# Kernel tuning notes

Measured on AMD Instinct MI355X. Metric: run time of the kernel, lower is better.

The kernel has to match this reference:

```python
import jax, jax.numpy as jnp
import numpy as np

N = 50000      # graph nodes
E = 400000     # random edges (plus N self-loops)
F = 128        # graph feature dim
H = 4          # GAT heads (layer1)
DH = 64        # gnn_hidden_size (per-head out, layer1)
EMB = 8        # emb_size / GAT final out
B = 16384      # batch
NS = 20        # number of sparse features
V = 1000       # vocab per sparse feature
DENSE = 64     # num_fea_size
HID = 256      # hidden_dims
EPS = 1e-5


def setup_inputs():
    key = jax.random.key(0)
    ks = jax.random.split(key, 40)
    loop = jnp.arange(N, dtype=jnp.int32)
    src = jnp.concatenate([jax.random.randint(ks[0], (E,), 0, N, dtype=jnp.int32), loop])
    dst = jnp.concatenate([jax.random.randint(ks[1], (E,), 0, N, dtype=jnp.int32), loop])
    s = 0.05
    d = {
        'X_id': jax.random.randint(ks[2], (B, 2), 0, N),
        'X_sparse': jax.random.randint(ks[3], (B, NS), 0, V),
        'X_dense': jax.random.normal(ks[4], (B, DENSE), jnp.float32),
        'emb_tables': jax.random.normal(ks[5], (NS, V, EMB), jnp.float32) * s,
        'graph_feature': jax.random.normal(ks[6], (N, F), jnp.float32),
        'src': src, 'dst': dst,
        'wide_w': jax.random.normal(ks[7], (EMB, DENSE), jnp.float32) * s,
        'wide_b': jnp.zeros((EMB,), jnp.float32),
        'lin1_w': jax.random.normal(ks[8], (HID, NS * EMB + DENSE), jnp.float32) * s,
        'lin1_b': jnp.zeros((HID,), jnp.float32),
        'bn1_g': jnp.ones((HID,), jnp.float32),
        'bn1_b': jnp.zeros((HID,), jnp.float32),
        'bn1_m': jax.random.normal(ks[9], (HID,), jnp.float32) * s,
        'bn1_v': jnp.ones((HID,), jnp.float32),
        'lin2_w': jax.random.normal(ks[10], (HID, HID), jnp.float32) * s,
        'lin2_b': jnp.zeros((HID,), jnp.float32),
        'bn2_g': jnp.ones((HID,), jnp.float32),
        'bn2_b': jnp.zeros((HID,), jnp.float32),
        'bn2_m': jax.random.normal(ks[11], (HID,), jnp.float32) * s,
        'bn2_v': jnp.ones((HID,), jnp.float32),
        'dnn_w': jax.random.normal(ks[12], (EMB, HID), jnp.float32) * s,
        'dnn_b': jnp.zeros((EMB,), jnp.float32),
        'gat1_w': jax.random.normal(ks[13], (H * DH, F), jnp.float32) * s,
        'gat1_al': jax.random.normal(ks[14], (H, DH), jnp.float32) * s,
        'gat1_ar': jax.random.normal(ks[15], (H, DH), jnp.float32) * s,
        'gat1_bias': jnp.zeros((H * DH,), jnp.float32),
        'gat2_w': jax.random.normal(ks[16], (EMB, H * DH), jnp.float32) * s,
        'gat2_al': jax.random.normal(ks[17], (1, EMB), jnp.float32) * s,
        'gat2_ar': jax.random.normal(ks[18], (1, EMB), jnp.float32) * s,
        'gat2_bias': jnp.zeros((EMB,), jnp.float32),
        'g1w': jax.random.normal(ks[19], (1, EMB), jnp.float32) * s,
        'g1b': jnp.zeros((1,), jnp.float32),
        'g2w': jax.random.normal(ks[20], (1, EMB), jnp.float32) * s,
        'g2b': jnp.zeros((1,), jnp.float32),
        'g3w': jax.random.normal(ks[21], (1, EMB), jnp.float32) * s,
        'g3b': jnp.zeros((1,), jnp.float32),
        'gout_w': jax.random.normal(ks[22], (2, 3 * EMB), jnp.float32) * s,
        'gout_b': jnp.zeros((2,), jnp.float32),
    }
    return d


def gat_conv(h, W, al, ar, bias, src, dst, heads, dh):
    # DGL GATConv: project, per-edge attention, edge-softmax over dst, aggregate
    feat = (h @ W.T).reshape(-1, heads, dh)          # [N, H, D]
    el = (feat * al).sum(-1)                          # [N, H] src score
    er = (feat * ar).sum(-1)                          # [N, H] dst score
    e = jax.nn.leaky_relu(el[src] + er[dst], 0.2)     # [Etot, H]
    emax = jax.lax.stop_gradient(jax.ops.segment_max(e, dst, num_segments=N))
    a = jnp.exp(e - emax[dst])
    denom = jax.ops.segment_sum(a, dst, num_segments=N)  # [N, H]
    alpha = a / denom[dst]                            # [Etot, H]
    out = jax.ops.segment_sum(alpha[:, :, None] * feat[src], dst, num_segments=N)
    return out + bias.reshape(1, heads, dh)           # [N, H, D]


def batchnorm_eval(x, g, b, m, v):
    return g * (x - m) * jax.lax.rsqrt(v + EPS) + b


def reference(X_id, X_sparse, X_dense, emb_tables, graph_feature, src, dst,
              wide_w, wide_b, lin1_w, lin1_b, bn1_g, bn1_b, bn1_m, bn1_v,
              lin2_w, lin2_b, bn2_g, bn2_b, bn2_m, bn2_v, dnn_w, dnn_b,
              gat1_w, gat1_al, gat1_ar, gat1_bias, gat2_w, gat2_al, gat2_ar, gat2_bias,
              g1w, g1b, g2w, g2b, g3w, g3b, gout_w, gout_b):
    commit_ids = X_id[:, 1]
    # sparse embedding lookup: [B, NS, EMB] -> [B, NS*EMB]
    sparse_embed = emb_tables[jnp.arange(NS)[None, :], X_sparse].reshape(B, NS * EMB)
    x = jnp.concatenate([sparse_embed, X_dense], axis=-1)
    wide_out = X_dense @ wide_w.T + wide_b            # [B, EMB]
    # deep MLP (eval-mode BN, dropout = identity)
    d = jax.nn.relu(batchnorm_eval(x @ lin1_w.T + lin1_b, bn1_g, bn1_b, bn1_m, bn1_v))
    d = jax.nn.relu(batchnorm_eval(d @ lin2_w.T + lin2_b, bn2_g, bn2_b, bn2_m, bn2_v))
    deep_out = d @ dnn_w.T + dnn_b                    # [B, EMB]
    # GAT
    h1 = gat_conv(graph_feature, gat1_w, gat1_al, gat1_ar, gat1_bias, src, dst, H, DH)
    h1 = jax.nn.elu(h1.reshape(N, H * DH))
    h2 = gat_conv(h1, gat2_w, gat2_al, gat2_ar, gat2_bias, src, dst, 1, EMB)
    gcn = h2.reshape(N, EMB)                          # squeeze head dim
    gcn_out = gcn[commit_ids]                         # [B, EMB]
    # Gate (concat)
    aw = jax.nn.sigmoid(wide_out @ g1w.T + g1b)
    bw = jax.nn.sigmoid(deep_out @ g2w.T + g2b)
    cw = jax.nn.sigmoid(gcn_out @ g3w.T + g3b)
    tot = aw + bw + cw
    combined = jnp.concatenate([(aw / tot) * wide_out, (bw / tot) * deep_out,
                                (cw / tot) * gcn_out], axis=1)
    out = combined @ gout_w.T + gout_b                # [B, 2]
    return jax.nn.softmax(out, axis=1)
```

## Files before the change

kernel.cpp:

```cpp
#include <hip/hip_runtime.h>

#define TPB 256
#define DCAP 64
constexpr float BN_EPS = 1e-5f;

typedef __attribute__((ext_vector_type(8))) short short8;
typedef __attribute__((ext_vector_type(4))) float floatx4;

__device__ __forceinline__ float sigmoidf_(float x) { return 1.f / (1.f + __expf(-x)); }
__device__ __forceinline__ unsigned short f2bf(float f) {
    unsigned u = __float_as_uint(f);
    u += 0x7FFFu + ((u >> 16) & 1u);
    return (unsigned short)(u >> 16);
}
__device__ __forceinline__ float bf2f(unsigned short h) {
    return __uint_as_float((unsigned)h << 16);
}
__device__ __forceinline__ float bflo(unsigned v) { return __uint_as_float(v << 16); }
__device__ __forceinline__ float bfhi(unsigned v) { return __uint_as_float(v & 0xFFFF0000u); }

__device__ __forceinline__ void async_load16(const unsigned short* g, unsigned short* l) {
    __builtin_amdgcn_global_load_lds(
        (const __attribute__((address_space(1))) void*)g,
        (__attribute__((address_space(3))) void*)l, 16, 0, 0);
}

template<bool BNRELU, bool ATTN>
__device__ __forceinline__ void gemm_dev(
    const unsigned short* __restrict__ A, const unsigned short* __restrict__ W,
    const float* __restrict__ bias,
    const float* __restrict__ g, const float* __restrict__ bb,
    const float* __restrict__ bm, const float* __restrict__ bv,
    unsigned short* __restrict__ C, int M, int N, int K, int m0, int n0,
    unsigned short* As, unsigned short* Bs,
    const float* __restrict__ al = nullptr, const float* __restrict__ ar = nullptr,
    float* __restrict__ el = nullptr, float* __restrict__ er = nullptr)
{
    constexpr int SK = 32;
    int tid = threadIdx.x;
    int wave = tid >> 6, lane = tid & 63;
    int wm = (wave & 1) * 32, wn = (wave >> 1) * 32;
    int lrow = lane & 15, lk = (lane >> 4) * 8;
    int sr = tid >> 2, sc = (tid & 3) * 8;
    int gmA = m0 + sr; if (gmA >= M) gmA = M - 1;
    const unsigned short* gA = A + (size_t)gmA * K + sc;
    const unsigned short* gB = W + (size_t)(n0 + sr) * K + sc;
    unsigned short* lA = As + wave * 512;
    unsigned short* lB = Bs + wave * 512;
    floatx4 acc[2][2] = {};
    for (int k0 = 0; k0 < K; k0 += 32) {
        async_load16(gA + k0, lA);
        async_load16(gB + k0, lB);
        __syncthreads();
        short8 af[2], bfr[2];
#pragma unroll
        for (int i = 0; i < 2; ++i)
            af[i] = *(const short8*)(As + (wm + i * 16 + lrow) * SK + lk);
#pragma unroll
        for (int j = 0; j < 2; ++j)
            bfr[j] = *(const short8*)(Bs + (wn + j * 16 + lrow) * SK + lk);
#pragma unroll
        for (int i = 0; i < 2; ++i)
#pragma unroll
            for (int j = 0; j < 2; ++j)
                acc[i][j] = __builtin_amdgcn_mfma_f32_16x16x32_bf16(
                    af[i], bfr[j], acc[i][j], 0, 0, 0);
        __syncthreads();
    }
    int crow = (lane >> 4) * 4, ccol = lane & 15;
    float pl[2][4], pr[2][4];
    if (ATTN) {
#pragma unroll
        for (int i = 0; i < 2; ++i)
#pragma unroll
            for (int r = 0; r < 4; ++r) { pl[i][r] = 0.f; pr[i][r] = 0.f; }
    }
#pragma unroll
    for (int j = 0; j < 2; ++j) {
        int gn = n0 + wn + j * 16 + ccol;
        float sc2 = 1.f, sh = 0.f;
        if (BNRELU) {
            sc2 = g[gn] * rsqrtf(bv[gn] + BN_EPS);
            sh = (bias[gn] - bm[gn]) * sc2 + bb[gn];
        }
        float alv = 0.f, arv = 0.f;
        if (ATTN) { alv = al[gn]; arv = ar[gn]; }
#pragma unroll
        for (int i = 0; i < 2; ++i) {
#pragma unroll
            for (int r = 0; r < 4; ++r) {
                int gm = m0 + wm + i * 16 + crow + r;
                float t = acc[i][j][r];
                if (BNRELU) t = fmaxf(t * sc2 + sh, 0.f);
                unsigned short tb = f2bf(t);
                if (gm < M) C[(size_t)gm * N + gn] = tb;
                if (ATTN) {
                    float tf = bf2f(tb);
                    pl[i][r] += tf * alv;
                    pr[i][r] += tf * arv;
                }
            }
        }
    }
    if (ATTN) {
#pragma unroll
        for (int off = 1; off < 16; off <<= 1)
#pragma unroll
            for (int i = 0; i < 2; ++i)
#pragma unroll
                for (int r = 0; r < 4; ++r) {
                    pl[i][r] += __shfl_xor(pl[i][r], off, 16);
                    pr[i][r] += __shfl_xor(pr[i][r], off, 16);
                }
        float* scr = (float*)As;
        if (ccol == 0) {
#pragma unroll
            for (int i = 0; i < 2; ++i)
#pragma unroll
                for (int r = 0; r < 4; ++r) {
                    int row = wm + i * 16 + crow + r;
                    scr[(row * 2 + (wn >> 5)) * 2 + 0] = pl[i][r];
                    scr[(row * 2 + (wn >> 5)) * 2 + 1] = pr[i][r];
                }
        }
        __syncthreads();
        if (tid < 64) {
            int gm = m0 + tid;
            if (gm < M) {
                float e_l = scr[(tid * 2 + 0) * 2 + 0] + scr[(tid * 2 + 1) * 2 + 0];
                float e_r = scr[(tid * 2 + 0) * 2 + 1] + scr[(tid * 2 + 1) * 2 + 1];
                int h = n0 >> 6;
                el[(size_t)gm * 4 + h] = e_l;
                er[(size_t)gm * 4 + h] = e_r;
            }
        }
    }
}

__global__ __launch_bounds__(TPB) void stageA_kernel(
    const int* __restrict__ src, const int* __restrict__ dst,
    int* __restrict__ cnt, int* __restrict__ esrc, int E, int sblk,
    const float* __restrict__ w1, unsigned short* __restrict__ o1,
    const float* __restrict__ w2, unsigned short* __restrict__ o2,
    const float* __restrict__ w3, unsigned short* __restrict__ o3,
    const float* __restrict__ gfeat, unsigned short* __restrict__ gfeatb, int ng4,
    const int* __restrict__ Xs, const float* __restrict__ Xd,
    const float* __restrict__ emb, unsigned short* __restrict__ x, int nx, int pblk,
    const float* __restrict__ Ww, const float* __restrict__ wb,
    float* __restrict__ wide, int B)
{
    if ((int)blockIdx.x < sblk) {
        int i = blockIdx.x * TPB + threadIdx.x;
        if (i >= E) return;
        int d = dst[i];
        int pos = atomicAdd(&cnt[d], 1);
        if (pos < DCAP) esrc[(size_t)d * DCAP + pos] = src[i];
        return;
    }
    if ((int)blockIdx.x < sblk + pblk) {
        const int NW = 256 * 224 + 256 * 256 + 256 * 128;
        int idx = (blockIdx.x - sblk) * TPB + threadIdx.x;
        if (idx < NW) {
            if (idx < 256 * 224) o1[idx] = f2bf(w1[idx]);
            else if (idx < 256 * 224 + 256 * 256) o2[idx - 256 * 224] = f2bf(w2[idx - 256 * 224]);
            else o3[idx - 256 * 224 - 256 * 256] = f2bf(w3[idx - 256 * 224 - 256 * 256]);
            return;
        }
        int i = idx - NW;
        if (i < ng4) {
            float4 v = ((const float4*)gfeat)[i];
            ushort4 o;
            o.x = f2bf(v.x); o.y = f2bf(v.y); o.z = f2bf(v.z); o.w = f2bf(v.w);
            ((ushort4*)gfeatb)[i] = o;
            return;
        }
        i -= ng4;
        if (i >= nx) return;
        int b = i / 224, c = i - b * 224;
        float v;
        if (c < 160) {
            int s = c >> 3, j = c & 7;
            int e = Xs[b * 20 + s];
            v = emb[((size_t)s * 1000 + e) * 8 + j];
        } else {
            v = Xd[b * 64 + (c - 160)];
        }
        x[i] = f2bf(v);
        return;
    }
    int lane = threadIdx.x & 63;
    int r = (blockIdx.x - sblk - pblk) * 4 + (threadIdx.x >> 6);
    if (r >= B) return;
    float a = Xd[(size_t)r * 64 + lane];
    float p[8];
#pragma unroll
    for (int j = 0; j < 8; ++j) p[j] = a * Ww[j * 64 + lane];
#pragma unroll
    for (int off = 1; off < 64; off <<= 1)
#pragma unroll
        for (int j = 0; j < 8; ++j) p[j] += __shfl_xor(p[j], off, 64);
    if (lane == 0) {
#pragma unroll
        for (int j = 0; j < 8; ++j) wide[(size_t)r * 8 + j] = p[j] + wb[j];
    }
}

__global__ __launch_bounds__(256) void stageB_kernel(
    const unsigned short* __restrict__ xb, const unsigned short* __restrict__ w1b,
    const float* __restrict__ lin1_b,
    const float* __restrict__ bn1_g, const float* __restrict__ bn1_b,
    const float* __restrict__ bn1_m, const float* __restrict__ bn1_v,
    unsigned short* __restrict__ d1, int B, int mb1,
    const unsigned short* __restrict__ gfeatb, const unsigned short* __restrict__ wg1b,
    unsigned short* __restrict__ feat1, int Nn, int mbf,
    const float* __restrict__ al, const float* __restrict__ ar,
    float* __restrict__ el, float* __restrict__ er)
{
    __shared__ unsigned short As[64 * 32];
    __shared__ unsigned short Bs[64 * 32];
    int bid = blockIdx.x;
    int nblk1 = mb1 * 4;
    if (bid < nblk1) {
        int bx = bid % mb1, by = bid / mb1;
        gemm_dev<true, false>(xb, w1b, lin1_b, bn1_g, bn1_b, bn1_m, bn1_v,
                              d1, B, 256, 224, bx * 64, by * 64, As, Bs);
    } else {
        int b2 = bid - nblk1;
        int bx = b2 % mbf, by = b2 / mbf;
        gemm_dev<false, true>(gfeatb, wg1b, nullptr, nullptr, nullptr, nullptr, nullptr,
                              feat1, Nn, 256, 128, bx * 64, by * 64, As, Bs,
                              al, ar, el, er);
    }
}

__global__ __launch_bounds__(256) void stageC_kernel(
    const unsigned short* __restrict__ d1, const unsigned short* __restrict__ w2b,
    const float* __restrict__ lin2_b,
    const float* __restrict__ bn2_g, const float* __restrict__ bn2_b,
    const float* __restrict__ bn2_m, const float* __restrict__ bn2_v,
    unsigned short* __restrict__ d2, int B, int mb1)
{
    __shared__ unsigned short As[64 * 32];
    __shared__ unsigned short Bs[64 * 32];
    int bx = blockIdx.x % mb1, by = blockIdx.x / mb1;
    gemm_dev<true, false>(d1, w2b, lin2_b, bn2_g, bn2_b, bn2_m, bn2_v,
                          d2, B, 256, 256, bx * 64, by * 64, As, Bs);
}

__global__ __launch_bounds__(TPB) void stageD_kernel(
    const unsigned short* __restrict__ d2, const float* __restrict__ Wd,
    const float* __restrict__ db, float* __restrict__ deep, int B, int hblk,
    const unsigned short* __restrict__ feat, const float* __restrict__ el,
    const float* __restrict__ er, const int* __restrict__ cnt,
    const int* __restrict__ esrc, const float* __restrict__ bias,
    const float* __restrict__ w2g, const float* __restrict__ al2,
    const float* __restrict__ ar2,
    float* __restrict__ feat2, float* __restrict__ el2, float* __restrict__ er2, int Nn)
{
    int lane = threadIdx.x & 63;
    if ((int)blockIdx.x < hblk) {
        int r = blockIdx.x * 4 + (threadIdx.x >> 6);
        if (r >= B) return;
        float p[8];
        uint2 ab = *(const uint2*)(d2 + (size_t)r * 256 + lane * 4);
        float a0 = bflo(ab.x), a1 = bfhi(ab.x), a2 = bflo(ab.y), a3 = bfhi(ab.y);
#pragma unroll
        for (int j = 0; j < 8; ++j) {
            float4 wv = *(const float4*)(Wd + j * 256 + lane * 4);
            p[j] = a0 * wv.x + a1 * wv.y + a2 * wv.z + a3 * wv.w;
        }
#pragma unroll
        for (int off = 1; off < 64; off <<= 1)
#pragma unroll
            for (int j = 0; j < 8; ++j) p[j] += __shfl_xor(p[j], off, 64);
        if (lane == 0) {
#pragma unroll
            for (int j = 0; j < 8; ++j) deep[(size_t)r * 8 + j] = p[j] + db[j];
        }
        return;
    }
    int n = (blockIdx.x - hblk) * 4 + (threadIdx.x >> 6);
    if (n >= Nn) return;
    int h = lane >> 4;
    int c = h * 64 + (lane & 15) * 4;
    float erv = er[n * 4 + h];
    int beg = n * DCAP;
    int deg = cnt[n]; if (deg > DCAP) deg = DCAP;
    int end = beg + deg;
    float4 acc = make_float4(0.f, 0.f, 0.f, 0.f);
    float dsum = 0.f;
    int e = beg;
    for (; e + 4 <= end; e += 4) {
        int sv[4]; float lv[4]; uint2 fb[4];
#pragma unroll
        for (int u = 0; u < 4; ++u) sv[u] = esrc[e + u];
#pragma unroll
        for (int u = 0; u < 4; ++u) lv[u] = el[sv[u] * 4 + h];
#pragma unroll
        for (int u = 0; u < 4; ++u) fb[u] = *(const uint2*)(feat + (size_t)sv[u] * 256 + c);
#pragma unroll
        for (int u = 0; u < 4; ++u) {
            float ev = lv[u] + erv;
            ev = ev > 0.f ? ev : 0.2f * ev;
            float av = __expf(ev);
            dsum += av;
            acc.x += av * bflo(fb[u].x); acc.y += av * bfhi(fb[u].x);
            acc.z += av * bflo(fb[u].y); acc.w += av * bfhi(fb[u].y);
        }
    }
    for (; e < end; ++e) {
        int s = esrc[e];
        float ev = el[s * 4 + h] + erv;
        ev = ev > 0.f ? ev : 0.2f * ev;
        float av = __expf(ev);
        dsum += av;
        uint2 fb = *(const uint2*)(feat + (size_t)s * 256 + c);
        acc.x += av * bflo(fb.x); acc.y += av * bfhi(fb.x);
        acc.z += av * bflo(fb.y); acc.w += av * bfhi(fb.y);
    }
    float inv = 1.f / dsum;
    float4 bv = *(const float4*)(bias + c);
    float4 o;
    o.x = acc.x * inv + bv.x; o.y = acc.y * inv + bv.y;
    o.z = acc.z * inv + bv.z; o.w = acc.w * inv + bv.w;
    o.x = o.x > 0.f ? o.x : __expf(o.x) - 1.f;
    o.y = o.y > 0.f ? o.y : __expf(o.y) - 1.f;
    o.z = o.z > 0.f ? o.z : __expf(o.z) - 1.f;
    o.w = o.w > 0.f ? o.w : __expf(o.w) - 1.f;
    float p[8];
#pragma unroll
    for (int j = 0; j < 8; ++j) {
        float4 wv = *(const float4*)(w2g + j * 256 + c);
        p[j] = o.x * wv.x + o.y * wv.y + o.z * wv.z + o.w * wv.w;
    }
#pragma unroll
    for (int off = 1; off < 64; off <<= 1)
#pragma unroll
        for (int j = 0; j < 8; ++j)
            p[j] += __shfl_xor(p[j], off, 64);
    if (lane == 0) {
        float e_l = 0.f, e_r = 0.f;
#pragma unroll
        for (int j = 0; j < 8; ++j) {
            feat2[(size_t)n * 8 + j] = p[j];
            e_l += p[j] * al2[j];
            e_r += p[j] * ar2[j];
        }
        el2[n] = e_l; er2[n] = e_r;
    }
}

__global__ __launch_bounds__(TPB) void gat2_final_kernel(
    const float* __restrict__ feat2, const float* __restrict__ el,
    const float* __restrict__ er, const int* __restrict__ cnt,
    const int* __restrict__ esrc, const int* __restrict__ Xid,
    const float* __restrict__ wide, const float* __restrict__ deep,
    const float* __restrict__ g2bias,
    const float* __restrict__ g1w, const float* __restrict__ g1b,
    const float* __restrict__ g2w, const float* __restrict__ g2b,
    const float* __restrict__ g3w, const float* __restrict__ g3b,
    const float* __restrict__ goutw, const float* __restrict__ goutb,
    float* __restrict__ out, int B)
{
    __shared__ float ls[256];
    int tid = threadIdx.x;
    int b = blockIdx.x * 32 + (tid >> 3), j = tid & 7;
    if (b < B) {
        int n = Xid[b * 2 + 1];
        float erv = er[n];
        int beg = n * DCAP;
        int deg = cnt[n]; if (deg > DCAP) deg = DCAP;
        int end = beg + deg;
        float acc = 0.f, dsum = 0.f;
        int e = beg;
        for (; e + 4 <= end; e += 4) {
            int sv[4]; float lv[4], fv[4];
#pragma unroll
            for (int u = 0; u < 4; ++u) sv[u] = esrc[e + u];
#pragma unroll
            for (int u = 0; u < 4; ++u) lv[u] = el[sv[u]];
#pragma unroll
            for (int u = 0; u < 4; ++u) fv[u] = feat2[(size_t)sv[u] * 8 + j];
#pragma unroll
            for (int u = 0; u < 4; ++u) {
                float ev = lv[u] + erv;
                ev = ev > 0.f ? ev : 0.2f * ev;
                float av = __expf(ev);
                dsum += av;
                acc += av * fv[u];
            }
        }
        for (; e < end; ++e) {
            int s = esrc[e];
            float ev = el[s] + erv;
            ev = ev > 0.f ? ev : 0.2f * ev;
            float av = __expf(ev);
            dsum += av;
            acc += av * feat2[(size_t)s * 8 + j];
        }
        ls[tid] = acc / dsum + g2bias[j];
    }
    __syncthreads();
    if (tid >= 32) return;
    int br = blockIdx.x * 32 + tid;
    if (br >= B) return;
    float w8[8], d8[8], g8[8];
    {
        float4 t0 = *(const float4*)(wide + (size_t)br * 8);
        float4 t1 = *(const float4*)(wide + (size_t)br * 8 + 4);
        w8[0] = t0.x; w8[1] = t0.y; w8[2] = t0.z; w8[3] = t0.w;
        w8[4] = t1.x; w8[5] = t1.y; w8[6] = t1.z; w8[7] = t1.w;
        t0 = *(const float4*)(deep + (size_t)br * 8);
        t1 = *(const float4*)(deep + (size_t)br * 8 + 4);
        d8[0] = t0.x; d8[1] = t0.y; d8[2] = t0.z; d8[3] = t0.w;
        d8[4] = t1.x; d8[5] = t1.y; d8[6] = t1.z; d8[7] = t1.w;
#pragma unroll
        for (int j2 = 0; j2 < 8; ++j2) g8[j2] = ls[tid * 8 + j2];
    }
    float s1 = g1b[0], s2 = g2b[0], s3 = g3b[0];
#pragma unroll
    for (int j2 = 0; j2 < 8; ++j2) { s1 += w8[j2] * g1w[j2]; s2 += d8[j2] * g2w[j2]; s3 += g8[j2] * g3w[j2]; }
    float aw = sigmoidf_(s1), bw = sigmoidf_(s2), cw = sigmoidf_(s3);
    float inv_tot = 1.f / (aw + bw + cw);
    float an = aw * inv_tot, bn = bw * inv_tot, cn = cw * inv_tot;
    float o0 = goutb[0], o1 = goutb[1];
#pragma unroll
    for (int j2 = 0; j2 < 8; ++j2) {
        float c0 = an * w8[j2]; o0 += goutw[j2] * c0;      o1 += goutw[24 + j2] * c0;
        float c1 = bn * d8[j2]; o0 += goutw[8 + j2] * c1;  o1 += goutw[32 + j2] * c1;
        float c2 = cn * g8[j2]; o0 += goutw[16 + j2] * c2; o1 += goutw[40 + j2] * c2;
    }
    float mx = fmaxf(o0, o1);
    float e0 = __expf(o0 - mx), e1 = __expf(o1 - mx);
    float inv = 1.f / (e0 + e1);
    out[(size_t)br * 2] = e0 * inv;
    out[(size_t)br * 2 + 1] = e1 * inv;
}

extern "C" void kernel_launch(void* const* d_in, const int* in_sizes, int n_in,
                              void* d_out, int out_size, void* d_ws, size_t ws_size,
                              hipStream_t stream)
{
    const int*   Xid    = (const int*)d_in[0];
    const int*   Xs     = (const int*)d_in[1];
    const float* Xd     = (const float*)d_in[2];
    const float* emb    = (const float*)d_in[3];
    const float* gfeat  = (const float*)d_in[4];
    const int*   src    = (const int*)d_in[5];
    const int*   dst    = (const int*)d_in[6];
    const float* wide_w = (const float*)d_in[7];
    const float* wide_b = (const float*)d_in[8];
    const float* lin1_w = (const float*)d_in[9];
    const float* lin1_b = (const float*)d_in[10];
    const float* bn1_g  = (const float*)d_in[11];
    const float* bn1_b  = (const float*)d_in[12];
    const float* bn1_m  = (const float*)d_in[13];
    const float* bn1_v  = (const float*)d_in[14];
    const float* lin2_w = (const float*)d_in[15];
    const float* lin2_b = (const float*)d_in[16];
    const float* bn2_g  = (const float*)d_in[17];
    const float* bn2_b  = (const float*)d_in[18];
    const float* bn2_m  = (const float*)d_in[19];
    const float* bn2_v  = (const float*)d_in[20];
    const float* dnn_w  = (const float*)d_in[21];
    const float* dnn_b  = (const float*)d_in[22];
    const float* gat1_w = (const float*)d_in[23];
    const float* gat1_al = (const float*)d_in[24];
    const float* gat1_ar = (const float*)d_in[25];
    const float* gat1_bias = (const float*)d_in[26];
    const float* gat2_w = (const float*)d_in[27];
    const float* gat2_al = (const float*)d_in[28];
    const float* gat2_ar = (const float*)d_in[29];
    const float* gat2_bias = (const float*)d_in[30];
    const float* g1w = (const float*)d_in[31];
    const float* g1b = (const float*)d_in[32];
    const float* g2w = (const float*)d_in[33];
    const float* g2b = (const float*)d_in[34];
    const float* g3w = (const float*)d_in[35];
    const float* g3b = (const float*)d_in[36];
    const float* goutw = (const float*)d_in[37];
    const float* goutb = (const float*)d_in[38];

    const int B    = in_sizes[0] / 2;
    const int Nn   = in_sizes[4] / 128;
    const int Etot = in_sizes[5];

    char* base = (char*)d_ws;
    size_t off = 0;
    auto alloc = [&](size_t bytes) -> char* {
        char* p = base + off;
        off += (bytes + 255) & ~(size_t)255;
        return p;
    };
    unsigned short* xb = (unsigned short*)alloc((size_t)B * 224 * 2);
    unsigned short* d1 = (unsigned short*)alloc((size_t)B * 256 * 2);
    unsigned short* d2 = (unsigned short*)alloc((size_t)B * 256 * 2);
    unsigned short* feat1  = (unsigned short*)alloc((size_t)Nn * 256 * 2);
    unsigned short* gfeatb = (unsigned short*)alloc((size_t)Nn * 128 * 2);
    unsigned short* w1b = (unsigned short*)alloc(256 * 224 * 2);
    unsigned short* w2b = (unsigned short*)alloc(256 * 256 * 2);
    unsigned short* wg1b = (unsigned short*)alloc(256 * 128 * 2);
    float* wide  = (float*)alloc((size_t)B * 8 * 4);
    float* deep  = (float*)alloc((size_t)B * 8 * 4);
    float* el1   = (float*)alloc((size_t)Nn * 4 * 4);
    float* er1   = (float*)alloc((size_t)Nn * 4 * 4);
    float* feat2 = (float*)alloc((size_t)Nn * 8 * 4);
    float* el2   = (float*)alloc((size_t)Nn * 4);
    float* er2   = (float*)alloc((size_t)Nn * 4);
    int* cnt     = (int*)alloc((size_t)Nn * 4);
    int* esrc    = (int*)alloc((size_t)Nn * DCAP * 4);

    hipMemsetAsync(cnt, 0, (size_t)Nn * sizeof(int), stream);

    {
        const int sblk = (Etot + TPB - 1) / TPB;
        const int NW = 256 * 224 + 256 * 256 + 256 * 128;
        const int NG4 = Nn * 128 / 4;
        const int NX = B * 224;
        const int pblk = (NW + NG4 + NX + TPB - 1) / TPB;
        const int wblk = (B + 3) / 4;
        stageA_kernel<<<sblk + pblk + wblk, TPB, 0, stream>>>(
            src, dst, cnt, esrc, Etot, sblk,
            lin1_w, w1b, lin2_w, w2b, gat1_w, wg1b,
            gfeat, gfeatb, NG4, Xs, Xd, emb, xb, NX, pblk,
            wide_w, wide_b, wide, B);
    }

    const int mb1 = (B + 63) / 64;
    const int mbf = (Nn + 63) / 64;

    stageB_kernel<<<mb1 * 4 + mbf * 4, 256, 0, stream>>>(
        xb, w1b, lin1_b, bn1_g, bn1_b, bn1_m, bn1_v, d1, B, mb1,
        gfeatb, wg1b, feat1, Nn, mbf, gat1_al, gat1_ar, el1, er1);

    stageC_kernel<<<mb1 * 4, 256, 0, stream>>>(
        d1, w2b, lin2_b, bn2_g, bn2_b, bn2_m, bn2_v, d2, B, mb1);

    {
        const int hblk = (B + 3) / 4;
        const int gblk = (Nn + 3) / 4;
        stageD_kernel<<<hblk + gblk, TPB, 0, stream>>>(
            d2, dnn_w, dnn_b, deep, B, hblk,
            feat1, el1, er1, cnt, esrc, gat1_bias,
            gat2_w, gat2_al, gat2_ar, feat2, el2, er2, Nn);
    }

    gat2_final_kernel<<<(B + 31) / 32, TPB, 0, stream>>>(
        feat2, el2, er2, cnt, esrc, Xid, wide, deep, gat2_bias,
        g1w, g1b, g2w, g2b, g3w, g3b, goutw, goutb, (float*)d_out, B);
}
```

Before: 279.1 us.

## Merge lin2 GEMM with GAT1 aggregation, fold deep head into final kernel, 16-bit edge indices

Runs the lin2 GEMM blocks in the same launch as the GAT layer-1 aggregation blocks, so the two independent workloads overlap and one kernel launch disappears. The deep-output projection (256->8) moves into the final gating kernel, where each of 8 threads per row computes one output, which removes the deep buffer and another launch. Edge source indices are stored as 16-bit values to halve adjacency traffic. N is 50000, so indices fit in 16 bits, but any graph with more than 65535 nodes would silently produce wrong results.

```diff
diff --git a/kernel.cpp b/kernel.cpp
--- a/kernel.cpp
+++ b/kernel.cpp
@@ -139,7 +139,7 @@
 
 __global__ __launch_bounds__(TPB) void stageA_kernel(
     const int* __restrict__ src, const int* __restrict__ dst,
-    int* __restrict__ cnt, int* __restrict__ esrc, int E, int sblk,
+    int* __restrict__ cnt, unsigned short* __restrict__ esrc, int E, int sblk,
     const float* __restrict__ w1, unsigned short* __restrict__ o1,
     const float* __restrict__ w2, unsigned short* __restrict__ o2,
     const float* __restrict__ w3, unsigned short* __restrict__ o3,
@@ -154,7 +154,7 @@
         if (i >= E) return;
         int d = dst[i];
         int pos = atomicAdd(&cnt[d], 1);
-        if (pos < DCAP) esrc[(size_t)d * DCAP + pos] = src[i];
+        if (pos < DCAP) esrc[(size_t)d * DCAP + pos] = (unsigned short)src[i];
         return;
     }
     if ((int)blockIdx.x < sblk + pblk) {
@@ -233,7 +233,14 @@
     }
 }
 
-__global__ __launch_bounds__(256) void stageC_kernel(
+__global__ __launch_bounds__(TPB) void stageC_kernel(
+    const unsigned short* __restrict__ feat, const float* __restrict__ el,
+    const float* __restrict__ er, const int* __restrict__ cnt,
+    const unsigned short* __restrict__ esrc, const float* __restrict__ bias,
+    const float* __restrict__ w2g, const float* __restrict__ al2,
+    const float* __restrict__ ar2,
+    float* __restrict__ feat2, float* __restrict__ el2, float* __restrict__ er2,
+    int Nn, int gblk,
     const unsigned short* __restrict__ d1, const unsigned short* __restrict__ w2b,
     const float* __restrict__ lin2_b,
     const float* __restrict__ bn2_g, const float* __restrict__ bn2_b,
@@ -242,44 +249,15 @@
 {
     __shared__ unsigned short As[64 * 32];
     __shared__ unsigned short Bs[64 * 32];
-    int bx = blockIdx.x % mb1, by = blockIdx.x / mb1;
-    gemm_dev<true, false>(d1, w2b, lin2_b, bn2_g, bn2_b, bn2_m, bn2_v,
-                          d2, B, 256, 256, bx * 64, by * 64, As, Bs);
-}
-
-__global__ __launch_bounds__(TPB) void stageD_kernel(
-    const unsigned short* __restrict__ d2, const float* __restrict__ Wd,
-    const float* __restrict__ db, float* __restrict__ deep, int B, int hblk,
-    const unsigned short* __restrict__ feat, const float* __restrict__ el,
-    const float* __restrict__ er, const int* __restrict__ cnt,
-    const int* __restrict__ esrc, const float* __restrict__ bias,
-    const float* __restrict__ w2g, const float* __restrict__ al2,
-    const float* __restrict__ ar2,
-    float* __restrict__ feat2, float* __restrict__ el2, float* __restrict__ er2, int Nn)
-{
     int lane = threadIdx.x & 63;
-    if ((int)blockIdx.x < hblk) {
-        int r = blockIdx.x * 4 + (threadIdx.x >> 6);
-        if (r >= B) return;
-        float p[8];
-        uint2 ab = *(const uint2*)(d2 + (size_t)r * 256 + lane * 4);
-        float a0 = bflo(ab.x), a1 = bfhi(ab.x), a2 = bflo(ab.y), a3 = bfhi(ab.y);
-#pragma unroll
-        for (int j = 0; j < 8; ++j) {
-            float4 wv = *(const float4*)(Wd + j * 256 + lane * 4);
-            p[j] = a0 * wv.x + a1 * wv.y + a2 * wv.z + a3 * wv.w;
-        }
-#pragma unroll
-        for (int off = 1; off < 64; off <<= 1)
-#pragma unroll
-            for (int j = 0; j < 8; ++j) p[j] += __shfl_xor(p[j], off, 64);
-        if (lane == 0) {
-#pragma unroll
-            for (int j = 0; j < 8; ++j) deep[(size_t)r * 8 + j] = p[j] + db[j];
-        }
+    if ((int)blockIdx.x >= gblk) {
+        int b2 = blockIdx.x - gblk;
+        int bx = b2 % mb1, by = b2 / mb1;
+        gemm_dev<true, false>(d1, w2b, lin2_b, bn2_g, bn2_b, bn2_m, bn2_v,
+                              d2, B, 256, 256, bx * 64, by * 64, As, Bs);
         return;
     }
-    int n = (blockIdx.x - hblk) * 4 + (threadIdx.x >> 6);
+    int n = blockIdx.x * 4 + (threadIdx.x >> 6);
     if (n >= Nn) return;
     int h = lane >> 4;
     int c = h * 64 + (lane & 15) * 4;
@@ -350,11 +328,13 @@
     }
 }
 
-__global__ __launch_bounds__(TPB) void gat2_final_kernel(
+__global__ __launch_bounds__(TPB) void stageE_kernel(
+    const unsigned short* __restrict__ d2, const float* __restrict__ Wd,
+    const float* __restrict__ db,
     const float* __restrict__ feat2, const float* __restrict__ el,
     const float* __restrict__ er, const int* __restrict__ cnt,
-    const int* __restrict__ esrc, const int* __restrict__ Xid,
-    const float* __restrict__ wide, const float* __restrict__ deep,
+    const unsigned short* __restrict__ esrc, const int* __restrict__ Xid,
+    const float* __restrict__ wide,
     const float* __restrict__ g2bias,
     const float* __restrict__ g1w, const float* __restrict__ g1b,
     const float* __restrict__ g2w, const float* __restrict__ g2b,
@@ -363,9 +343,23 @@
     float* __restrict__ out, int B)
 {
     __shared__ float ls[256];
+    __shared__ float lsd[256];
     int tid = threadIdx.x;
     int b = blockIdx.x * 32 + (tid >> 3), j = tid & 7;
     if (b < B) {
+        {
+            const uint2* dp = (const uint2*)(d2 + (size_t)b * 256);
+            const float4* wp = (const float4*)(Wd + j * 256);
+            float s = db[j];
+#pragma unroll 8
+            for (int k = 0; k < 64; ++k) {
+                uint2 ab = dp[k];
+                float4 wv = wp[k];
+                s += bflo(ab.x) * wv.x + bfhi(ab.x) * wv.y
+                   + bflo(ab.y) * wv.z + bfhi(ab.y) * wv.w;
+            }
+            lsd[tid] = s;
+        }
         int n = Xid[b * 2 + 1];
         float erv = er[n];
         int beg = n * DCAP;
@@ -410,12 +404,8 @@
         float4 t1 = *(const float4*)(wide + (size_t)br * 8 + 4);
         w8[0] = t0.x; w8[1] = t0.y; w8[2] = t0.z; w8[3] = t0.w;
         w8[4] = t1.x; w8[5] = t1.y; w8[6] = t1.z; w8[7] = t1.w;
-        t0 = *(const float4*)(deep + (size_t)br * 8);
-        t1 = *(const float4*)(deep + (size_t)br * 8 + 4);
-        d8[0] = t0.x; d8[1] = t0.y; d8[2] = t0.z; d8[3] = t0.w;
-        d8[4] = t1.x; d8[5] = t1.y; d8[6] = t1.z; d8[7] = t1.w;
-#pragma unroll
-        for (int j2 = 0; j2 < 8; ++j2) g8[j2] = ls[tid * 8 + j2];
+#pragma unroll
+        for (int j2 = 0; j2 < 8; ++j2) { d8[j2] = lsd[tid * 8 + j2]; g8[j2] = ls[tid * 8 + j2]; }
     }
     float s1 = g1b[0], s2 = g2b[0], s3 = g3b[0];
 #pragma unroll
@@ -501,14 +491,13 @@
     unsigned short* w2b = (unsigned short*)alloc(256 * 256 * 2);
     unsigned short* wg1b = (unsigned short*)alloc(256 * 128 * 2);
     float* wide  = (float*)alloc((size_t)B * 8 * 4);
-    float* deep  = (float*)alloc((size_t)B * 8 * 4);
     float* el1   = (float*)alloc((size_t)Nn * 4 * 4);
     float* er1   = (float*)alloc((size_t)Nn * 4 * 4);
     float* feat2 = (float*)alloc((size_t)Nn * 8 * 4);
     float* el2   = (float*)alloc((size_t)Nn * 4);
     float* er2   = (float*)alloc((size_t)Nn * 4);
     int* cnt     = (int*)alloc((size_t)Nn * 4);
-    int* esrc    = (int*)alloc((size_t)Nn * DCAP * 4);
+    unsigned short* esrc = (unsigned short*)alloc((size_t)Nn * DCAP * 2);
 
     hipMemsetAsync(cnt, 0, (size_t)Nn * sizeof(int), stream);
 
@@ -533,19 +522,15 @@
         xb, w1b, lin1_b, bn1_g, bn1_b, bn1_m, bn1_v, d1, B, mb1,
         gfeatb, wg1b, feat1, Nn, mbf, gat1_al, gat1_ar, el1, er1);
 
-    stageC_kernel<<<mb1 * 4, 256, 0, stream>>>(
-        d1, w2b, lin2_b, bn2_g, bn2_b, bn2_m, bn2_v, d2, B, mb1);
-
     {
-        const int hblk = (B + 3) / 4;
         const int gblk = (Nn + 3) / 4;
-        stageD_kernel<<<hblk + gblk, TPB, 0, stream>>>(
-            d2, dnn_w, dnn_b, deep, B, hblk,
+        stageC_kernel<<<gblk + mb1 * 4, TPB, 0, stream>>>(
             feat1, el1, er1, cnt, esrc, gat1_bias,
-            gat2_w, gat2_al, gat2_ar, feat2, el2, er2, Nn);
-    }
-
-    gat2_final_kernel<<<(B + 31) / 32, TPB, 0, stream>>>(
-        feat2, el2, er2, cnt, esrc, Xid, wide, deep, gat2_bias,
+            gat2_w, gat2_al, gat2_ar, feat2, el2, er2, Nn, gblk,
+            d1, w2b, lin2_b, bn2_g, bn2_b, bn2_m, bn2_v, d2, B, mb1);
+    }
+
+    stageE_kernel<<<(B + 31) / 32, TPB, 0, stream>>>(
+        d2, dnn_w, dnn_b, feat2, el2, er2, cnt, esrc, Xid, wide, gat2_bias,
         g1w, g1b, g2w, g2b, g3w, g3b, goutw, goutb, (float*)d_out, B);
 }
```

Measured after the change: 289.9 us. 1.04x slower.
